# Kernel tuning notes

Measured on AMD Instinct MI355X. Metric: run time of the kernel, lower is better.

## Reference

```python
import jax, jax.numpy as jnp
import numpy as np
from jax import lax

H = 1024
E = 8
TOP_K = 2


def setup_inputs() -> dict:
    key = jax.random.key(0)
    kx, k1, k2 = jax.random.split(key, 3)
    x = jax.random.normal(kx, (8, 2048, H), dtype=jnp.float32)
    # router MLP params, init normal(0, 0.02), zero bias (matches _init_weights)
    w1 = jax.random.normal(k1, (H, 2 * H), dtype=jnp.float32) * 0.02
    b1 = jnp.zeros((2 * H,), dtype=jnp.float32)
    w2 = jax.random.normal(k2, (2 * H, E), dtype=jnp.float32) * 0.02
    b2 = jnp.zeros((E,), dtype=jnp.float32)
    return {"x": x, "w1": w1, "b1": b1, "w2": w2, "b2": b2}


def reference(x, w1, b1, w2, b2):
    # gating MLP: Linear -> GELU (exact, torch default) -> Linear
    h = jax.nn.gelu(jnp.einsum('bsh,hf->bsf', x, w1) + b1, approximate=False)
    expert_weights = jnp.einsum('bsf,fe->bse', h, w2) + b2  # [B,S,E]

    top_k_weights, top_k_indices = lax.top_k(expert_weights, TOP_K)  # [B,S,K]
    top_k_weights = jax.nn.softmax(top_k_weights, axis=-1)

    # scatter renormalized weights into dense [B,S,E] mask (indices distinct -> one-hot sum)
    onehot = jax.nn.one_hot(top_k_indices, E, dtype=expert_weights.dtype)  # [B,S,K,E]
    masks = jnp.einsum('bsk,bske->bse', top_k_weights, onehot)

    expert_usage = masks.sum(axis=(0, 1))
    expert_usage = expert_usage / expert_usage.sum()
    target_usage = jnp.full_like(expert_usage, 1.0 / E)
    load_balancing_loss = jnp.mean((expert_usage - target_usage) ** 2)

    sparsity_loss = jnp.mean(jnp.sum(masks > 0, axis=-1).astype(jnp.float32)) / TOP_K
    total_loss = load_balancing_loss + 0.1 * sparsity_loss

    return expert_weights, masks, total_loss, expert_usage
```

## Files before the change

kernel.cpp:

```cpp
#include <hip/hip_runtime.h>
#include <math.h>

#define HDIM 1024
#define FDIM 2048
#define NEXP 8
#define MTOK 16384
#define NSLC 32
#define ROWS 2048
#define BM 128
#define BN 128

typedef __attribute__((ext_vector_type(8))) short bf16x8;
typedef __attribute__((ext_vector_type(4))) float f32x4;

__device__ inline unsigned short f2bf_rne(float f) {
    unsigned int u = __float_as_uint(f);
    u = (u + 0x7FFFu + ((u >> 16) & 1u)) >> 16;
    return (unsigned short)u;
}
__device__ inline float bf2f(unsigned short h) {
    unsigned int u = ((unsigned int)h) << 16;
    return __uint_as_float(u);
}

__global__ __launch_bounds__(256) void cvt_x(const float* __restrict__ x,
                                             unsigned short* __restrict__ xi)
{
    size_t g = (size_t)blockIdx.x * 256 + threadIdx.x;
    size_t m = g >> 7, k8 = g & 127;
    const float* p = x + g * 8;
    float v[8];
    *(float4*)(v)     = *(const float4*)(p);
    *(float4*)(v + 4) = *(const float4*)(p + 4);
    union { unsigned short u[8]; uint4 q; } oh, ol;
    #pragma unroll
    for (int j = 0; j < 8; j++) {
        unsigned short h = f2bf_rne(v[j]);
        oh.u[j] = h;
        ol.u[j] = f2bf_rne(v[j] - bf2f(h));
    }
    unsigned short* dst = xi + m * ROWS + k8 * 16;
    *(uint4*)dst = oh.q;
    *(uint4*)(dst + 8) = ol.q;
}

__global__ __launch_bounds__(256) void cvt_w1f(const float* __restrict__ w1,
                                               unsigned short* __restrict__ wf)
{
    __shared__ float t[32][33];
    int n0 = blockIdx.x * 32;
    int k0 = blockIdx.y * 32;
    int lx = threadIdx.x & 31, ly = threadIdx.x >> 5;
    #pragma unroll
    for (int r = 0; r < 32; r += 8)
        t[ly + r][lx] = w1[(size_t)(k0 + ly + r) * FDIM + n0 + lx];
    __syncthreads();
    #pragma unroll
    for (int r = 0; r < 32; r += 8) {
        float v = t[lx][ly + r];
        unsigned short h = f2bf_rne(v);
        unsigned short l = f2bf_rne(v - bf2f(h));
        int n = n0 + ly + r, k = k0 + lx;
        size_t base = (size_t)((n >> 4) * 32 + (k >> 5)) * 1024;
        int lj = (((k >> 3) & 3) * 16 + (n & 15)) * 8 + (k & 7);
        wf[base + lj] = h;
        wf[base + 512 + lj] = l;
    }
}

__global__ __launch_bounds__(256, 2) void gemm1_mfma(
    const unsigned short* __restrict__ xi, const unsigned short* __restrict__ wf,
    const float* __restrict__ b1, const float* __restrict__ w2,
    float* __restrict__ part)
{
    __shared__ __align__(16) short As[2][BM * 64];

    const int tid  = threadIdx.x;
    const int lane = tid & 63;
    const int l15  = lane & 15;
    const int q    = lane >> 4;
    const int wave = tid >> 6;
    const int wm   = wave & 1;
    const int wn   = wave >> 1;
    const int bm = blockIdx.x, bn = blockIdx.y;
    const int m0 = bm * BM, n0 = bn * BN;

    const unsigned short* ap[4];
    #pragma unroll
    for (int s = 0; s < 4; s++) {
        int c = s * 256 + tid;
        int m = c >> 3;
        int g = (c & 7) ^ (m & 7);
        ap[s] = xi + (size_t)(m0 + m) * ROWS + g * 8;
    }

    const unsigned short* bq[4][2];
    #pragma unroll
    for (int f = 0; f < 4; f++) {
        int nt = bn * 8 + wn * 4 + f;
        #pragma unroll
        for (int h = 0; h < 2; h++)
            bq[f][h] = wf + (size_t)nt * 32768 + h * 512 + lane * 8;
    }

    int offA[2][4];
    #pragma unroll
    for (int i = 0; i < 4; i++) {
        int ma = wm * 64 + i * 16 + l15;
        offA[0][i] = (ma * 8 + ((2 * q)     ^ (ma & 7))) * 8;
        offA[1][i] = (ma * 8 + ((2 * q + 1) ^ (ma & 7))) * 8;
    }

    f32x4 acc[4][4];
    #pragma unroll
    for (int i = 0; i < 4; i++)
        #pragma unroll
        for (int j = 0; j < 4; j++) acc[i][j] = (f32x4){0.f, 0.f, 0.f, 0.f};

    #pragma unroll
    for (int s = 0; s < 4; s++)
        __builtin_amdgcn_global_load_lds(
            (const __attribute__((address_space(1))) void*)(ap[s]),
            (__attribute__((address_space(3))) void*)&As[0][(s * 256 + tid) * 8],
            16, 0, 0);

    for (int t = 0; t < 32; t++) {
        __syncthreads();

        bf16x8 bh[4], bl[4];
        #pragma unroll
        for (int f = 0; f < 4; f++) {
            bh[f] = *(const bf16x8*)(bq[f][0] + t * 1024);
            bl[f] = *(const bf16x8*)(bq[f][1] + t * 1024);
        }
        if (t + 1 < 32) {
            const int nbuf = (t + 1) & 1;
            #pragma unroll
            for (int s = 0; s < 4; s++)
                __builtin_amdgcn_global_load_lds(
                    (const __attribute__((address_space(1))) void*)(ap[s] + (t + 1) * 64),
                    (__attribute__((address_space(3))) void*)&As[nbuf][(s * 256 + tid) * 8],
                    16, 0, 0);
        }

        const short* a = As[t & 1];
        bf16x8 ah[4], al[4];
        #pragma unroll
        for (int i = 0; i < 4; i++) {
            ah[i] = *(const bf16x8*)&a[offA[0][i]];
            al[i] = *(const bf16x8*)&a[offA[1][i]];
        }
        #pragma unroll
        for (int i = 0; i < 4; i++)
            #pragma unroll
            for (int j = 0; j < 4; j++) {
                acc[i][j] = __builtin_amdgcn_mfma_f32_16x16x32_bf16(
                    ah[i], bh[j], acc[i][j], 0, 0, 0);
                acc[i][j] = __builtin_amdgcn_mfma_f32_16x16x32_bf16(
                    ah[i], bl[j], acc[i][j], 0, 0, 0);
                acc[i][j] = __builtin_amdgcn_mfma_f32_16x16x32_bf16(
                    al[i], bh[j], acc[i][j], 0, 0, 0);
            }
    }

    #pragma unroll
    for (int j = 0; j < 4; j++) {
        int n = n0 + wn * 64 + j * 16 + l15;
        float bb = b1[n];
        #pragma unroll
        for (int i = 0; i < 4; i++)
            #pragma unroll
            for (int r = 0; r < 4; r++) {
                float v = acc[i][j][r] + bb;
                acc[i][j][r] = 0.5f * v * (1.0f + erff(v * 0.70710678118654752f));
            }
    }

    float w2r[4][8];
    #pragma unroll
    for (int j = 0; j < 4; j++) {
        const float4* p = (const float4*)(w2 + (size_t)(n0 + wn * 64 + j * 16 + l15) * NEXP);
        float4 u = p[0], v = p[1];
        w2r[j][0] = u.x; w2r[j][1] = u.y; w2r[j][2] = u.z; w2r[j][3] = u.w;
        w2r[j][4] = v.x; w2r[j][5] = v.y; w2r[j][6] = v.z; w2r[j][7] = v.w;
    }

    const int sl = bn * 2 + wn;
    #pragma unroll
    for (int e = 0; e < NEXP; e++) {
        float p[4][4];
        #pragma unroll
        for (int i = 0; i < 4; i++)
            #pragma unroll
            for (int r = 0; r < 4; r++) {
                float s = 0.f;
                #pragma unroll
                for (int j = 0; j < 4; j++) s += acc[i][j][r] * w2r[j][e];
                p[i][r] = s;
            }
        #pragma unroll
        for (int off = 1; off < 16; off <<= 1)
            #pragma unroll
            for (int i = 0; i < 4; i++)
                #pragma unroll
                for (int r = 0; r < 4; r++)
                    p[i][r] += __shfl_xor(p[i][r], off);
        if (l15 == 0) {
            #pragma unroll
            for (int i = 0; i < 4; i++)
                #pragma unroll
                for (int r = 0; r < 4; r++) {
                    int m = m0 + wm * 64 + i * 16 + q * 4 + r;
                    part[(size_t)sl * (MTOK * NEXP) + (size_t)m * NEXP + e] = p[i][r];
                }
        }
    }
}

__global__ __launch_bounds__(256) void router_topk(
    const float* __restrict__ part, const float* __restrict__ b2,
    float* __restrict__ out, float* __restrict__ gu, int* __restrict__ gc)
{
    const int t = blockIdx.x * 256 + threadIdx.x;

    float logit[8];
    #pragma unroll
    for (int e = 0; e < 8; e++) logit[e] = b2[e];
    #pragma unroll
    for (int j = 0; j < NSLC; j++) {
        const float4* p4 = (const float4*)(part + (size_t)j * (MTOK * NEXP) + (size_t)t * NEXP);
        float4 u = p4[0], v = p4[1];
        logit[0] += u.x; logit[1] += u.y; logit[2] += u.z; logit[3] += u.w;
        logit[4] += v.x; logit[5] += v.y; logit[6] += v.z; logit[7] += v.w;
    }

    int i1 = 0; float v1 = logit[0];
    #pragma unroll
    for (int e = 1; e < 8; e++) { if (logit[e] > v1) { v1 = logit[e]; i1 = e; } }
    int i2 = -1; float v2 = -INFINITY;
    #pragma unroll
    for (int e = 0; e < 8; e++) {
        if (e != i1 && logit[e] > v2) { v2 = logit[e]; i2 = e; }
    }
    float ex = expf(v2 - v1);
    float inv = 1.0f / (1.0f + ex);
    float wa = inv, wb = ex * inv;

    float4* o = (float4*)(out + (size_t)t * NEXP);
    o[0] = make_float4(logit[0], logit[1], logit[2], logit[3]);
    o[1] = make_float4(logit[4], logit[5], logit[6], logit[7]);

    float mk[8];
    #pragma unroll
    for (int e = 0; e < 8; e++) mk[e] = 0.0f;
    mk[i1] = wa; mk[i2] = wb;
    float4* om = (float4*)(out + (size_t)(MTOK * NEXP) + (size_t)t * NEXP);
    om[0] = make_float4(mk[0], mk[1], mk[2], mk[3]);
    om[1] = make_float4(mk[4], mk[5], mk[6], mk[7]);

    __shared__ float us[8];
    __shared__ int cs;
    if (threadIdx.x < 8) us[threadIdx.x] = 0.0f;
    if (threadIdx.x == 0) cs = 0;
    __syncthreads();
    atomicAdd(&us[i1], wa);
    atomicAdd(&us[i2], wb);
    int cnt = (wa > 0.0f ? 1 : 0) + (wb > 0.0f ? 1 : 0);
    atomicAdd(&cs, cnt);
    __syncthreads();
    if (threadIdx.x < 8) atomicAdd(&gu[threadIdx.x], us[threadIdx.x]);
    if (threadIdx.x == 0) atomicAdd(gc, cs);
}

__global__ void router_final(const float* __restrict__ gu, const int* __restrict__ gc,
                             float* __restrict__ out)
{
    if (blockIdx.x == 0 && threadIdx.x == 0) {
        float u[8]; float tot = 0.0f;
        for (int e = 0; e < 8; e++) { u[e] = gu[e]; tot += u[e]; }
        float lb = 0.0f;
        for (int e = 0; e < 8; e++) {
            float un = u[e] / tot;
            out[2 * MTOK * NEXP + 1 + e] = un;
            float d = un - 0.125f;
            lb += d * d;
        }
        lb *= (1.0f / 8.0f);
        float sp = ((float)(*gc) / (float)MTOK) * 0.5f;
        out[2 * MTOK * NEXP] = lb + 0.1f * sp;
    }
}

extern "C" void kernel_launch(void* const* d_in, const int* in_sizes, int n_in,
                              void* d_out, int out_size, void* d_ws, size_t ws_size,
                              hipStream_t stream) {
    const float* x  = (const float*)d_in[0];
    const float* w1 = (const float*)d_in[1];
    const float* b1 = (const float*)d_in[2];
    const float* w2 = (const float*)d_in[3];
    const float* b2 = (const float*)d_in[4];
    float* out = (float*)d_out;

    unsigned short* xi = (unsigned short*)d_ws;
    unsigned short* wf = xi + (size_t)MTOK * ROWS;
    float* part = (float*)(wf + (size_t)128 * 32 * 1024);
    float* gu = part + (size_t)NSLC * MTOK * NEXP;
    int* gc = (int*)(gu + 8);

    hipMemsetAsync(gu, 0, 64, stream);

    cvt_x<<<(MTOK * HDIM / 8) / 256, 256, 0, stream>>>(x, xi);
    cvt_w1f<<<dim3(FDIM / 32, HDIM / 32), 256, 0, stream>>>(w1, wf);
    gemm1_mfma<<<dim3(MTOK / BM, FDIM / BN), 256, 0, stream>>>(xi, wf, b1, w2, part);
    router_topk<<<MTOK / 256, 256, 0, stream>>>(part, b2, out, gu, gc);
    router_final<<<1, 64, 0, stream>>>(gu, gc, out);
}
```

Before: 351.6 us.

## Pre-tile activations into MFMA fragment layout and drop LDS staging in GEMM

The x conversion kernel now writes hi/lo bf16 activations in the same per-16-row fragment-tiled layout as the weights, so the GEMM can load A fragments straight from global memory into registers. The LDS double buffer and per-step barriers go away, replaced by a register double buffer that prefetches the next K step for both A and B. Blocks are remapped onto a 1D grid with an XCD-aware swizzle so neighbouring M tiles share an XCD's L2. The trade-offs are more register pressure and A reuse that now depends on L2 hits rather than LDS.

```diff
diff --git a/kernel.cpp b/kernel.cpp
--- a/kernel.cpp
+++ b/kernel.cpp
@@ -6,7 +6,6 @@
 #define NEXP 8
 #define MTOK 16384
 #define NSLC 32
-#define ROWS 2048
 #define BM 128
 #define BN 128
 
@@ -24,24 +23,43 @@
 }
 
 __global__ __launch_bounds__(256) void cvt_x(const float* __restrict__ x,
-                                             unsigned short* __restrict__ xi)
-{
-    size_t g = (size_t)blockIdx.x * 256 + threadIdx.x;
-    size_t m = g >> 7, k8 = g & 127;
-    const float* p = x + g * 8;
-    float v[8];
-    *(float4*)(v)     = *(const float4*)(p);
-    *(float4*)(v + 4) = *(const float4*)(p + 4);
-    union { unsigned short u[8]; uint4 q; } oh, ol;
-    #pragma unroll
-    for (int j = 0; j < 8; j++) {
-        unsigned short h = f2bf_rne(v[j]);
-        oh.u[j] = h;
-        ol.u[j] = f2bf_rne(v[j] - bf2f(h));
-    }
-    unsigned short* dst = xi + m * ROWS + k8 * 16;
-    *(uint4*)dst = oh.q;
-    *(uint4*)(dst + 8) = ol.q;
+                                             unsigned short* __restrict__ af)
+{
+    __shared__ unsigned short hs[16384];
+    __shared__ unsigned short ls[16384];
+    const int mt = blockIdx.x;
+    const float* src = x + (size_t)mt * 16384;
+    const int m = threadIdx.x & 15;
+    const int kseg = threadIdx.x >> 4;
+
+    #pragma unroll
+    for (int c = 0; c < 8; c++) {
+        int k = c * 128 + kseg * 8;
+        float v[8];
+        *(float4*)(v)     = *(const float4*)(src + m * 1024 + k);
+        *(float4*)(v + 4) = *(const float4*)(src + m * 1024 + k + 4);
+        union { unsigned short u[8]; uint4 q; } oh, ol;
+        #pragma unroll
+        for (int j = 0; j < 8; j++) {
+            unsigned short h = f2bf_rne(v[j]);
+            oh.u[j] = h;
+            ol.u[j] = f2bf_rne(v[j] - bf2f(h));
+        }
+        int kb = k >> 5, q = (k >> 3) & 3;
+        int o = kb * 512 + m * 32 + q * 8;
+        *(uint4*)(hs + o) = oh.q;
+        *(uint4*)(ls + o) = ol.q;
+    }
+    __syncthreads();
+    unsigned short* dst = af + (size_t)mt * 32768;
+    #pragma unroll
+    for (int c = 0; c < 16; c++) {
+        int f = c * 2048 + threadIdx.x * 8;
+        int kb = f >> 10, half = (f >> 9) & 1, idx = f & 511;
+        int q = idx >> 7, mm = (idx >> 3) & 15;
+        const unsigned short* s = (half ? ls : hs) + kb * 512 + mm * 32 + q * 8;
+        *(uint4*)(dst + f) = *(const uint4*)s;
+    }
 }
 
 __global__ __launch_bounds__(256) void cvt_w1f(const float* __restrict__ w1,
@@ -69,12 +87,10 @@
 }
 
 __global__ __launch_bounds__(256, 2) void gemm1_mfma(
-    const unsigned short* __restrict__ xi, const unsigned short* __restrict__ wf,
+    const unsigned short* __restrict__ af, const unsigned short* __restrict__ wf,
     const float* __restrict__ b1, const float* __restrict__ w2,
     float* __restrict__ part)
 {
-    __shared__ __align__(16) short As[2][BM * 64];
-
     const int tid  = threadIdx.x;
     const int lane = tid & 63;
     const int l15  = lane & 15;
@@ -82,33 +98,21 @@
     const int wave = tid >> 6;
     const int wm   = wave & 1;
     const int wn   = wave >> 1;
-    const int bm = blockIdx.x, bn = blockIdx.y;
+
+    const int id = blockIdx.x;
+    const int xcd = id & 7, seq = id >> 3;
+    const int strip = seq >> 6;
+    const int bn = (seq >> 2) & 15;
+    const int bmo = seq & 3;
+    const int bm = strip * 32 + xcd * 4 + bmo;
     const int m0 = bm * BM, n0 = bn * BN;
 
-    const unsigned short* ap[4];
-    #pragma unroll
-    for (int s = 0; s < 4; s++) {
-        int c = s * 256 + tid;
-        int m = c >> 3;
-        int g = (c & 7) ^ (m & 7);
-        ap[s] = xi + (size_t)(m0 + m) * ROWS + g * 8;
-    }
-
-    const unsigned short* bq[4][2];
-    #pragma unroll
-    for (int f = 0; f < 4; f++) {
-        int nt = bn * 8 + wn * 4 + f;
-        #pragma unroll
-        for (int h = 0; h < 2; h++)
-            bq[f][h] = wf + (size_t)nt * 32768 + h * 512 + lane * 8;
-    }
-
-    int offA[2][4];
+    const unsigned short* apt[4];
+    const unsigned short* bpt[4];
     #pragma unroll
     for (int i = 0; i < 4; i++) {
-        int ma = wm * 64 + i * 16 + l15;
-        offA[0][i] = (ma * 8 + ((2 * q)     ^ (ma & 7))) * 8;
-        offA[1][i] = (ma * 8 + ((2 * q + 1) ^ (ma & 7))) * 8;
+        apt[i] = af + ((size_t)(bm * 8 + wm * 4 + i) * 32) * 1024 + lane * 8;
+        bpt[i] = wf + ((size_t)(bn * 8 + wn * 4 + i) * 32) * 1024 + lane * 8;
     }
 
     f32x4 acc[4][4];
@@ -117,49 +121,58 @@
         #pragma unroll
         for (int j = 0; j < 4; j++) acc[i][j] = (f32x4){0.f, 0.f, 0.f, 0.f};
 
-    #pragma unroll
-    for (int s = 0; s < 4; s++)
-        __builtin_amdgcn_global_load_lds(
-            (const __attribute__((address_space(1))) void*)(ap[s]),
-            (__attribute__((address_space(3))) void*)&As[0][(s * 256 + tid) * 8],
-            16, 0, 0);
-
-    for (int t = 0; t < 32; t++) {
-        __syncthreads();
-
-        bf16x8 bh[4], bl[4];
-        #pragma unroll
-        for (int f = 0; f < 4; f++) {
-            bh[f] = *(const bf16x8*)(bq[f][0] + t * 1024);
-            bl[f] = *(const bf16x8*)(bq[f][1] + t * 1024);
-        }
-        if (t + 1 < 32) {
-            const int nbuf = (t + 1) & 1;
-            #pragma unroll
-            for (int s = 0; s < 4; s++)
-                __builtin_amdgcn_global_load_lds(
-                    (const __attribute__((address_space(1))) void*)(ap[s] + (t + 1) * 64),
-                    (__attribute__((address_space(3))) void*)&As[nbuf][(s * 256 + tid) * 8],
-                    16, 0, 0);
-        }
-
-        const short* a = As[t & 1];
-        bf16x8 ah[4], al[4];
+    bf16x8 Ah0[4], Al0[4], Bh0[4], Bl0[4];
+    bf16x8 Ah1[4], Al1[4], Bh1[4], Bl1[4];
+
+    #pragma unroll
+    for (int i = 0; i < 4; i++) {
+        Ah0[i] = *(const bf16x8*)(apt[i]);
+        Al0[i] = *(const bf16x8*)(apt[i] + 512);
+        Bh0[i] = *(const bf16x8*)(bpt[i]);
+        Bl0[i] = *(const bf16x8*)(bpt[i] + 512);
+    }
+
+    #pragma unroll 1
+    for (int t = 0; t < 32; t += 2) {
         #pragma unroll
         for (int i = 0; i < 4; i++) {
-            ah[i] = *(const bf16x8*)&a[offA[0][i]];
-            al[i] = *(const bf16x8*)&a[offA[1][i]];
+            Ah1[i] = *(const bf16x8*)(apt[i] + 1024);
+            Al1[i] = *(const bf16x8*)(apt[i] + 1536);
+            Bh1[i] = *(const bf16x8*)(bpt[i] + 1024);
+            Bl1[i] = *(const bf16x8*)(bpt[i] + 1536);
         }
         #pragma unroll
         for (int i = 0; i < 4; i++)
             #pragma unroll
             for (int j = 0; j < 4; j++) {
                 acc[i][j] = __builtin_amdgcn_mfma_f32_16x16x32_bf16(
-                    ah[i], bh[j], acc[i][j], 0, 0, 0);
-                acc[i][j] = __builtin_amdgcn_mfma_f32_16x16x32_bf16(
-                    ah[i], bl[j], acc[i][j], 0, 0, 0);
-                acc[i][j] = __builtin_amdgcn_mfma_f32_16x16x32_bf16(
-                    al[i], bh[j], acc[i][j], 0, 0, 0);
+                    Ah0[i], Bh0[j], acc[i][j], 0, 0, 0);
+                acc[i][j] = __builtin_amdgcn_mfma_f32_16x16x32_bf16(
+                    Ah0[i], Bl0[j], acc[i][j], 0, 0, 0);
+                acc[i][j] = __builtin_amdgcn_mfma_f32_16x16x32_bf16(
+                    Al0[i], Bh0[j], acc[i][j], 0, 0, 0);
+            }
+        #pragma unroll
+        for (int i = 0; i < 4; i++) { apt[i] += 2048; bpt[i] += 2048; }
+        if (t + 2 < 32) {
+            #pragma unroll
+            for (int i = 0; i < 4; i++) {
+                Ah0[i] = *(const bf16x8*)(apt[i]);
+                Al0[i] = *(const bf16x8*)(apt[i] + 512);
+                Bh0[i] = *(const bf16x8*)(bpt[i]);
+                Bl0[i] = *(const bf16x8*)(bpt[i] + 512);
+            }
+        }
+        #pragma unroll
+        for (int i = 0; i < 4; i++)
+            #pragma unroll
+            for (int j = 0; j < 4; j++) {
+                acc[i][j] = __builtin_amdgcn_mfma_f32_16x16x32_bf16(
+                    Ah1[i], Bh1[j], acc[i][j], 0, 0, 0);
+                acc[i][j] = __builtin_amdgcn_mfma_f32_16x16x32_bf16(
+                    Ah1[i], Bl1[j], acc[i][j], 0, 0, 0);
+                acc[i][j] = __builtin_amdgcn_mfma_f32_16x16x32_bf16(
+                    Al1[i], Bh1[j], acc[i][j], 0, 0, 0);
             }
     }
 
@@ -301,17 +314,17 @@
     const float* b2 = (const float*)d_in[4];
     float* out = (float*)d_out;
 
-    unsigned short* xi = (unsigned short*)d_ws;
-    unsigned short* wf = xi + (size_t)MTOK * ROWS;
+    unsigned short* af = (unsigned short*)d_ws;
+    unsigned short* wf = af + (size_t)1024 * 32768;
     float* part = (float*)(wf + (size_t)128 * 32 * 1024);
     float* gu = part + (size_t)NSLC * MTOK * NEXP;
     int* gc = (int*)(gu + 8);
 
     hipMemsetAsync(gu, 0, 64, stream);
 
-    cvt_x<<<(MTOK * HDIM / 8) / 256, 256, 0, stream>>>(x, xi);
+    cvt_x<<<1024, 256, 0, stream>>>(x, af);
     cvt_w1f<<<dim3(FDIM / 32, HDIM / 32), 256, 0, stream>>>(w1, wf);
-    gemm1_mfma<<<dim3(MTOK / BM, FDIM / BN), 256, 0, stream>>>(xi, wf, b1, w2, part);
+    gemm1_mfma<<<2048, 256, 0, stream>>>(af, wf, b1, w2, part);
     router_topk<<<MTOK / 256, 256, 0, stream>>>(part, b2, out, gu, gc);
     router_final<<<1, 64, 0, stream>>>(gu, gc, out);
 }
```

Result: no change. 345.8 us (-1.7%).
